# Kernel optimization log

Measured on AMD Instinct MI355X. Metric: run time of the kernel, lower is better.

## Reference

```python
import jax, jax.numpy as jnp
import numpy as np

B, L, C, H = 2, 4096, 512, 8
DH = C // H


def setup_inputs() -> dict:
    key = jax.random.key(0)
    ks = jax.random.split(key, 6)
    s = 1.0 / np.sqrt(C)
    return {
        "x": jax.random.normal(ks[0], (B, L, C), dtype=jnp.float32),
        "Wq": jax.random.normal(ks[1], (C, C), dtype=jnp.float32) * s,
        "Wk": jax.random.normal(ks[2], (C, C), dtype=jnp.float32) * s,
        "Wv": jax.random.normal(ks[3], (C, C), dtype=jnp.float32) * s,
        "Wo": jax.random.normal(ks[4], (C, C), dtype=jnp.float32) * s,
        "bo": jnp.zeros((C,), dtype=jnp.float32),
    }


def reference(x, Wq, Wk, Wv, Wo, bo):
    # x: [B, L, C]; split heads -> [B, H, L, Dh]
    def heads(t):
        return t.reshape(B, L, H, DH).transpose(0, 2, 1, 3)

    q = heads(x @ Wq)
    k = heads(x @ Wk)
    v = heads(x @ Wv)
    scale = 1.0 / np.sqrt(DH)
    scores = jnp.einsum("bhqd,bhkd->bhqk", q, k) * scale  # [B,H,L,L]
    w = jax.nn.softmax(scores, axis=-1)  # dropout_rate=0.0 -> identity
    att = jnp.einsum("bhqk,bhkd->bhqd", w, v)  # [B,H,L,Dh]
    att = att.transpose(0, 2, 1, 3).reshape(B, L, C)
    return att @ Wo + bo
```

## Files before the change

kernel.cpp:

```cpp
#include <hip/hip_runtime.h>
#include <hip/hip_bf16.h>

typedef __hip_bfloat16 bh;
typedef __attribute__((ext_vector_type(8))) __bf16 bf16x8;
typedef __attribute__((ext_vector_type(4))) float f32x4;
typedef __attribute__((ext_vector_type(4))) int i32x4;
typedef __attribute__((ext_vector_type(4))) short s16x4;

#define NB 2
#define NL 4096
#define NC 512
#define NH 8
#define NDH 64
#define NM (NB * NL)
#define LOG2E 1.4426950408889634f
#define KVBLK 8192

static __device__ __forceinline__ f32x4 mfma_bf16(bf16x8 a, bf16x8 b, f32x4 c) {
    return __builtin_amdgcn_mfma_f32_16x16x32_bf16(a, b, c, 0, 0, 0);
}
static __device__ __forceinline__ f32x4 mfma16(s16x4 a, s16x4 b, f32x4 c) {
    return __builtin_amdgcn_mfma_f32_16x16x16bf16_1k(a, b, c, 0, 0, 0);
}

static __device__ __forceinline__ void st_bf4(bh* dst, float a, float b, float c, float d) {
    bh tmp[4] = {__float2bfloat16(a), __float2bfloat16(b),
                 __float2bfloat16(c), __float2bfloat16(d)};
    *(s16x4*)dst = *(const s16x4*)tmp;
}
static __device__ __forceinline__ s16x4 pk_bf4(float a, float b, float c, float d) {
    bh tmp[4] = {__float2bfloat16(a), __float2bfloat16(b),
                 __float2bfloat16(c), __float2bfloat16(d)};
    return *(const s16x4*)tmp;
}

static __device__ __forceinline__ void gload16(const bh* g, bh* l) {
    __builtin_amdgcn_global_load_lds(
        (const __attribute__((address_space(1))) void*)g,
        (__attribute__((address_space(3))) void*)l,
        16, 0, 0);
}

__global__ __launch_bounds__(256, 2)
void prep(const float* __restrict__ x,
          const float* __restrict__ Wq, const float* __restrict__ Wk,
          const float* __restrict__ Wv, const float* __restrict__ Wo,
          bh* __restrict__ xf, bh* __restrict__ Wf)
{
    const int t = threadIdx.x;
    const int wave = t >> 6, lane = t & 63;
    const int quad = lane >> 4, c16 = lane & 15;

    if (blockIdx.z < 8) {
        __shared__ __align__(16) bh T[64][72];
        const int m64 = blockIdx.x, k64 = blockIdx.z;
        #pragma unroll
        for (int rep = 0; rep < 4; rep++) {
            int li = t + rep * 256;
            int r = li >> 4, c4 = (li & 15) * 4;
            float4 f = *(const float4*)&x[(size_t)(m64 * 64 + r) * 512 + k64 * 64 + c4];
            st_bf4(&T[r][c4], f.x, f.y, f.z, f.w);
        }
        __syncthreads();
        #pragma unroll
        for (int kcl = 0; kcl < 2; kcl++) {
            i32x4 v = *(const i32x4*)&T[wave * 16 + c16][kcl * 32 + quad * 8];
            size_t addr = ((size_t)(m64 * 4 + wave) * 16 + (k64 * 2 + kcl)) * 512 + lane * 8;
            *(i32x4*)&xf[addr] = v;
        }
    } else {
        if (blockIdx.x >= 64) return;
        int task = blockIdx.x * 4 + wave;
        int z = task >> 6, nt = (task >> 3) & 7, k0i = task & 7;
        const float* W = (z == 0) ? Wq : (z == 1) ? Wk : (z == 2) ? Wv : Wo;
        bh* dst = Wf + (((size_t)z * 8 + nt) * 8 + k0i) * 4096;
        #pragma unroll
        for (int kc = 0; kc < 2; kc++)
            #pragma unroll
            for (int fn = 0; fn < 4; fn++) {
                bh tmp[8];
                #pragma unroll
                for (int j = 0; j < 8; j++)
                    tmp[j] = __float2bfloat16(
                        W[(size_t)(k0i * 64 + kc * 32 + quad * 8 + j) * 512
                          + nt * 64 + fn * 16 + c16]);
                *(i32x4*)&dst[(kc * 4 + fn) * 512 + lane * 8] = *(const i32x4*)tmp;
            }
    }
}

__global__ __launch_bounds__(256, 2)
void qkv_gemm(const bh* __restrict__ xf, const bh* __restrict__ Wf,
              bh* __restrict__ Qb, bh* __restrict__ KVf)
{
    __shared__ __align__(16) bh smem[2][20480];

    const int t = threadIdx.x;
    const int wave = t >> 6, lane = t & 63;
    const int quad = lane >> 4, c16 = lane & 15;
    const int m0 = blockIdx.x * 128;
    const int nt = blockIdx.y;
    const int m16b = m0 >> 4;

    f32x4 acc[3][2][4];
    for (int z = 0; z < 3; z++)
        for (int a = 0; a < 2; a++)
            for (int b = 0; b < 4; b++)
                for (int u = 0; u < 4; u++) acc[z][a][b][u] = 0.0f;

    auto stage = [&](int k0i, int buf) {
        bh* Xl = &smem[buf][0];
        bh* Wl = &smem[buf][8192];
        #pragma unroll
        for (int r = 0; r < 4; r++) {
            int f = wave * 4 + r;
            const bh* src = xf + ((size_t)(m16b + (f >> 1)) * 16 + k0i * 2 + (f & 1)) * 512
                          + lane * 8;
            gload16(src, &Xl[f * 512 + lane * 8]);
        }
        #pragma unroll
        for (int z = 0; z < 3; z++) {
            const bh* wz = Wf + (((size_t)z * 8 + nt) * 8 + k0i) * 4096;
            #pragma unroll
            for (int r = 0; r < 2; r++) {
                int off = (wave * 2 + r) * 512 + lane * 8;
                gload16(wz + off, &Wl[z * 4096 + off]);
            }
        }
    };

    stage(0, 0);
    for (int k0i = 0; k0i < 8; k0i++) {
        const int buf = k0i & 1;
        __syncthreads();
        if (k0i < 7) stage(k0i + 1, buf ^ 1);
        const bh* Xl = &smem[buf][0];
        const bh* Wl = &smem[buf][8192];
        #pragma unroll
        for (int kc = 0; kc < 2; kc++) {
            bf16x8 af0 = *(const bf16x8*)&Xl[((wave * 2 + 0) * 2 + kc) * 512 + lane * 8];
            bf16x8 af1 = *(const bf16x8*)&Xl[((wave * 2 + 1) * 2 + kc) * 512 + lane * 8];
            #pragma unroll
            for (int z = 0; z < 3; z++)
                #pragma unroll
                for (int fn = 0; fn < 4; fn++) {
                    bf16x8 bf = *(const bf16x8*)&Wl[z * 4096 + (kc * 4 + fn) * 512 + lane * 8];
                    acc[z][0][fn] = mfma_bf16(af0, bf, acc[z][0][fn]);
                    acc[z][1][fn] = mfma_bf16(af1, bf, acc[z][1][fn]);
                }
        }
        __syncthreads();
    }

    const int h = nt;
    const int b = m0 >> 12;
    const int l0 = m0 & 4095;
    const int bh_i = b * NH + h;
    const int kt0 = l0 >> 6;

    {
        bh* Tq = &smem[0][0];
        #pragma unroll
        for (int fm = 0; fm < 2; fm++)
            #pragma unroll
            for (int i = 0; i < 4; i++) {
                int ll = wave * 32 + fm * 16 + quad * 4 + i;
                #pragma unroll
                for (int fn = 0; fn < 4; fn++)
                    Tq[ll * 68 + fn * 16 + c16] =
                        __float2bfloat16(acc[0][fm][fn][i] * 0.125f);
            }
        __syncthreads();
        int l = t >> 1, half = t & 1;
        bh* dst = Qb + ((size_t)bh_i * NL + l0 + l) * NDH + half * 32;
        const bh* src = &Tq[l * 68 + half * 32];
        #pragma unroll
        for (int r = 0; r < 4; r++)
            *(i32x4*)(dst + r * 8) = *(const i32x4*)(src + r * 8);
        __syncthreads();
    }

    {
        bh* Tk = &smem[0][0];
        #pragma unroll
        for (int fm = 0; fm < 2; fm++)
            #pragma unroll
            for (int i = 0; i < 4; i++) {
                int ll = wave * 32 + fm * 16 + quad * 4 + i;
                int ktl = ll >> 6, l64 = ll & 63;
                int fk = l64 >> 4, c16t = l64 & 15;
                #pragma unroll
                for (int fn = 0; fn < 4; fn++) {
                    int d = fn * 16 + c16;
                    int kc = d >> 5, qt = (d >> 3) & 3, j = d & 7;
                    Tk[ktl * 4096 + (fk * 2 + kc) * 512 + (qt * 16 + c16t) * 8 + j] =
                        __float2bfloat16(acc[1][fm][fn][i] * LOG2E);
                }
            }
        __syncthreads();
        int idx = t * 32;
        int ktl = idx >> 12, wi = idx & 4095;
        bh* dst = KVf + (size_t)(bh_i * 64 + kt0 + ktl) * KVBLK + wi;
        #pragma unroll
        for (int r = 0; r < 4; r++)
            *(i32x4*)(dst + r * 8) = *(const i32x4*)&Tk[idx + r * 8];
    }

    #pragma unroll
    for (int fm = 0; fm < 2; fm++) {
        int fkv = (wave * 2 + fm) & 3;
        int ktv = kt0 + (wave >> 1);
        #pragma unroll
        for (int fn = 0; fn < 4; fn++) {
            size_t addr = (size_t)(bh_i * 64 + ktv) * KVBLK + 4096
                        + (size_t)(fn * 4 + fkv) * 256 + (quad * 16 + c16) * 4;
            st_bf4(&KVf[addr], acc[2][fm][fn][0], acc[2][fm][fn][1],
                               acc[2][fm][fn][2], acc[2][fm][fn][3]);
        }
    }
}

__global__ __launch_bounds__(512, 4)
void flash_attn(const bh* __restrict__ Qb, const bh* __restrict__ KVf,
                bh* __restrict__ attb)
{
    __shared__ __align__(16) bh SF[2][2][KVBLK];

    const int t = threadIdx.x;
    const int wave = t >> 6, lane = t & 63;
    const int group = wave >> 2, w4 = wave & 3;
    const int quad = lane >> 4, c16 = lane & 15;
    const int bh_idx = blockIdx.y;
    const int q0 = blockIdx.x * 128;

    const bh* Qp  = Qb + (size_t)bh_idx * NL * NDH;
    const bh* KVp = KVf + (size_t)bh_idx * 64 * KVBLK;

    bf16x8 qf[2][2];
    #pragma unroll
    for (int fq = 0; fq < 2; fq++)
        #pragma unroll
        for (int kc = 0; kc < 2; kc++)
            qf[fq][kc] = *(const bf16x8*)
                &Qp[(size_t)(q0 + w4 * 32 + fq * 16 + c16) * NDH + kc * 32 + quad * 8];

    f32x4 ot[4][2];
    float lsum[2] = {0.0f, 0.0f};
    for (int a = 0; a < 4; a++)
        for (int fq = 0; fq < 2; fq++)
            for (int u = 0; u < 4; u++) ot[a][fq][u] = 0.0f;
    const f32x4 z4 = {0.0f, 0.0f, 0.0f, 0.0f};

    auto stage = [&](int i, int buf) {
        int kt = 2 * i + group;
        #pragma unroll
        for (int r = 0; r < 4; r++) {
            int off = (w4 * 4 + r) * 512 + lane * 8;
            gload16(KVp + (size_t)kt * KVBLK + off, &SF[group][buf][off]);
        }
    };

    stage(0, 0);
    for (int i = 0; i < 32; i++) {
        const int buf = i & 1;
        __syncthreads();
        if (i < 31) stage(i + 1, buf ^ 1);
        const bh* sf = &SF[group][buf][0];

        f32x4 s[4][2];
        #pragma unroll
        for (int fk = 0; fk < 4; fk++) {
            bf16x8 kf0 = *(const bf16x8*)&sf[(fk * 2 + 0) * 512 + lane * 8];
            s[fk][0] = mfma_bf16(kf0, qf[0][0], z4);
            s[fk][1] = mfma_bf16(kf0, qf[1][0], z4);
        }
        #pragma unroll
        for (int fk = 0; fk < 4; fk++) {
            bf16x8 kf1 = *(const bf16x8*)&sf[(fk * 2 + 1) * 512 + lane * 8];
            s[fk][0] = mfma_bf16(kf1, qf[0][1], s[fk][0]);
            s[fk][1] = mfma_bf16(kf1, qf[1][1], s[fk][1]);
        }

        s16x4 vt[4][4];
        #pragma unroll
        for (int fn = 0; fn < 4; fn++)
            #pragma unroll
            for (int fk = 0; fk < 4; fk++)
                vt[fn][fk] = *(const s16x4*)&sf[4096 + (fn * 4 + fk) * 256 + lane * 4];

        s16x4 pf[4][2];
        float rs0 = 0.0f, rs1 = 0.0f;
        #pragma unroll
        for (int fk = 0; fk < 4; fk++) {
            float a0 = __builtin_amdgcn_exp2f(s[fk][0][0]);
            float a1 = __builtin_amdgcn_exp2f(s[fk][0][1]);
            float a2 = __builtin_amdgcn_exp2f(s[fk][0][2]);
            float a3 = __builtin_amdgcn_exp2f(s[fk][0][3]);
            rs0 += (a0 + a1) + (a2 + a3);
            pf[fk][0] = pk_bf4(a0, a1, a2, a3);
            float b0 = __builtin_amdgcn_exp2f(s[fk][1][0]);
            float b1 = __builtin_amdgcn_exp2f(s[fk][1][1]);
            float b2 = __builtin_amdgcn_exp2f(s[fk][1][2]);
            float b3 = __builtin_amdgcn_exp2f(s[fk][1][3]);
            rs1 += (b0 + b1) + (b2 + b3);
            pf[fk][1] = pk_bf4(b0, b1, b2, b3);
        }
        lsum[0] += rs0;
        lsum[1] += rs1;

        #pragma unroll
        for (int fk = 0; fk < 4; fk++)
            #pragma unroll
            for (int fn = 0; fn < 4; fn++) {
                ot[fn][0] = mfma16(vt[fn][fk], pf[fk][0], ot[fn][0]);
                ot[fn][1] = mfma16(vt[fn][fk], pf[fk][1], ot[fn][1]);
            }
    }

    #pragma unroll
    for (int fq = 0; fq < 2; fq++) {
        lsum[fq] += __shfl_xor(lsum[fq], 16);
        lsum[fq] += __shfl_xor(lsum[fq], 32);
    }

    float* Ocmb = (float*)&SF[0][0][0];
    float* Lcmb = Ocmb + 128 * 64;
    __syncthreads();
    if (group == 1) {
        #pragma unroll
        for (int fq = 0; fq < 2; fq++) {
            int q = w4 * 32 + fq * 16 + c16;
            #pragma unroll
            for (int fn = 0; fn < 4; fn++)
                *(f32x4*)&Ocmb[q * 64 + fn * 16 + quad * 4] = ot[fn][fq];
            if (quad == 0) Lcmb[q] = lsum[fq];
        }
    }
    __syncthreads();
    if (group == 0) {
        const int b = bh_idx >> 3, h = bh_idx & 7;
        const int mbase16 = (b * NL + q0) >> 4;
        #pragma unroll
        for (int fq = 0; fq < 2; fq++) {
            int q = w4 * 32 + fq * 16 + c16;
            float inv = 1.0f / (lsum[fq] + Lcmb[q]);
            int m16 = mbase16 + w4 * 2 + fq;
            #pragma unroll
            for (int fn = 0; fn < 4; fn++) {
                f32x4 o2 = *(const f32x4*)&Ocmb[q * 64 + fn * 16 + quad * 4];
                size_t addr = ((size_t)m16 * 16 + h * 2 + (fn >> 1)) * 512
                            + (size_t)(((fn & 1) * 2 + (quad >> 1)) * 16 + c16) * 8
                            + (quad & 1) * 4;
                st_bf4(&attb[addr],
                       (ot[fn][fq][0] + o2[0]) * inv, (ot[fn][fq][1] + o2[1]) * inv,
                       (ot[fn][fq][2] + o2[2]) * inv, (ot[fn][fq][3] + o2[3]) * inv);
            }
        }
    }
}

__global__ __launch_bounds__(256, 2)
void out_gemm(const bh* __restrict__ Af, const bh* __restrict__ Wf,
              const float* __restrict__ bo, float* __restrict__ out)
{
    __shared__ __align__(16) bh smem[2][12288];

    const int t = threadIdx.x;
    const int wave = t >> 6, lane = t & 63;
    const int quad = lane >> 4, c16 = lane & 15;
    const int m0 = blockIdx.x * 128;
    const int nt = blockIdx.y;
    const int n0 = nt * 64;
    const int m16b = m0 >> 4;

    f32x4 acc[2][4];
    for (int a = 0; a < 2; a++)
        for (int b = 0; b < 4; b++)
            for (int u = 0; u < 4; u++) acc[a][b][u] = 0.0f;

    auto stage = [&](int k0i, int buf) {
        bh* Xl = &smem[buf][0];
        bh* Wl = &smem[buf][8192];
        #pragma unroll
        for (int r = 0; r < 4; r++) {
            int f = wave * 4 + r;
            const bh* src = Af + ((size_t)(m16b + (f >> 1)) * 16 + k0i * 2 + (f & 1)) * 512
                          + lane * 8;
            gload16(src, &Xl[f * 512 + lane * 8]);
        }
        const bh* wz = Wf + (((size_t)3 * 8 + nt) * 8 + k0i) * 4096;
        #pragma unroll
        for (int r = 0; r < 2; r++) {
            int off = (wave * 2 + r) * 512 + lane * 8;
            gload16(wz + off, &Wl[off]);
        }
    };

    stage(0, 0);
    for (int k0i = 0; k0i < 8; k0i++) {
        const int buf = k0i & 1;
        __syncthreads();
        if (k0i < 7) stage(k0i + 1, buf ^ 1);
        const bh* Xl = &smem[buf][0];
        const bh* Wl = &smem[buf][8192];
        #pragma unroll
        for (int kc = 0; kc < 2; kc++) {
            bf16x8 af0 = *(const bf16x8*)&Xl[((wave * 2 + 0) * 2 + kc) * 512 + lane * 8];
            bf16x8 af1 = *(const bf16x8*)&Xl[((wave * 2 + 1) * 2 + kc) * 512 + lane * 8];
            #pragma unroll
            for (int fn = 0; fn < 4; fn++) {
                bf16x8 bf = *(const bf16x8*)&Wl[(kc * 4 + fn) * 512 + lane * 8];
                acc[0][fn] = mfma_bf16(af0, bf, acc[0][fn]);
                acc[1][fn] = mfma_bf16(af1, bf, acc[1][fn]);
            }
        }
        __syncthreads();
    }

    #pragma unroll
    for (int fm = 0; fm < 2; fm++)
        #pragma unroll
        for (int i = 0; i < 4; i++) {
            int mr = m0 + wave * 32 + fm * 16 + quad * 4 + i;
            #pragma unroll
            for (int fn = 0; fn < 4; fn++) {
                int cn = n0 + fn * 16 + c16;
                out[(size_t)mr * 512 + cn] = acc[fm][fn][i] + bo[cn];
            }
        }
}

extern "C" void kernel_launch(void* const* d_in, const int* in_sizes, int n_in,
                              void* d_out, int out_size, void* d_ws, size_t ws_size,
                              hipStream_t stream)
{
    const float* x  = (const float*)d_in[0];
    const float* Wq = (const float*)d_in[1];
    const float* Wk = (const float*)d_in[2];
    const float* Wv = (const float*)d_in[3];
    const float* Wo = (const float*)d_in[4];
    const float* bo = (const float*)d_in[5];
    float* out = (float*)d_out;

    const size_t mat = (size_t)NM * NC;
    bh* Qb   = (bh*)d_ws;
    bh* KVf  = Qb + mat;
    bh* attb = KVf + 2 * mat;
    bh* Wf   = attb + mat;
    bh* xf   = Wf + 4 * 8 * 8 * 4096;

    prep      <<<dim3(128, 1, 9),         256, 0, stream>>>(x, Wq, Wk, Wv, Wo, xf, Wf);
    qkv_gemm  <<<dim3(NM / 128, NC / 64), 256, 0, stream>>>(xf, Wf, Qb, KVf);
    flash_attn<<<dim3(NL / 128, NB * NH), 512, 0, stream>>>(Qb, KVf, attb);
    out_gemm  <<<dim3(NM / 128, NC / 64), 256, 0, stream>>>(attb, Wf, bo, out);
}
```

Measured before the change: 186.5 us.

## Software-pipeline QK and PV across iterations with split K/V staging

Restructures the flash attention main loop so the PV MFMAs for tile i-1 interleave with the QK MFMAs and exp of tile i. K and V are now staged separately with their own double buffers, V loaded one iteration later than K, and P fragments ping-pong between two register sets. Wave priority is raised around the compute sections. This aims to hide exp/VALU latency behind MFMA work and shorten the serial dependency chain, at the cost of more live registers and a more complex prologue and epilogue.

```diff
diff --git a/kernel.cpp b/kernel.cpp
--- a/kernel.cpp
+++ b/kernel.cpp
@@ -224,7 +224,7 @@
 void flash_attn(const bh* __restrict__ Qb, const bh* __restrict__ KVf,
                 bh* __restrict__ attb)
 {
-    __shared__ __align__(16) bh SF[2][2][KVBLK];
+    __shared__ __align__(16) bh SMEM[32768];
 
     const int t = threadIdx.x;
     const int wave = t >> 6, lane = t & 63;
@@ -236,6 +236,9 @@
     const bh* Qp  = Qb + (size_t)bh_idx * NL * NDH;
     const bh* KVp = KVf + (size_t)bh_idx * 64 * KVBLK;
 
+    bh* Kb = &SMEM[group * 8192];
+    bh* Vb = &SMEM[16384 + group * 8192];
+
     bf16x8 qf[2][2];
     #pragma unroll
     for (int fq = 0; fq < 2; fq++)
@@ -251,70 +254,93 @@
             for (int u = 0; u < 4; u++) ot[a][fq][u] = 0.0f;
     const f32x4 z4 = {0.0f, 0.0f, 0.0f, 0.0f};
 
-    auto stage = [&](int i, int buf) {
+    s16x4 pfA[4][2], pfB[4][2];
+
+    auto stageK = [&](int i) {
         int kt = 2 * i + group;
-        #pragma unroll
-        for (int r = 0; r < 4; r++) {
-            int off = (w4 * 4 + r) * 512 + lane * 8;
-            gload16(KVp + (size_t)kt * KVBLK + off, &SF[group][buf][off]);
+        const bh* src = KVp + (size_t)kt * KVBLK;
+        bh* dst = Kb + (i & 1) * 4096;
+        #pragma unroll
+        for (int r = 0; r < 2; r++) {
+            int off = (w4 * 2 + r) * 512 + lane * 8;
+            gload16(src + off, dst + off);
         }
     };
-
-    stage(0, 0);
-    for (int i = 0; i < 32; i++) {
-        const int buf = i & 1;
-        __syncthreads();
-        if (i < 31) stage(i + 1, buf ^ 1);
-        const bh* sf = &SF[group][buf][0];
-
-        f32x4 s[4][2];
+    auto stageV = [&](int i) {
+        int kt = 2 * i + group;
+        const bh* src = KVp + (size_t)kt * KVBLK + 4096;
+        bh* dst = Vb + (i & 1) * 4096;
+        #pragma unroll
+        for (int r = 0; r < 2; r++) {
+            int off = (w4 * 2 + r) * 512 + lane * 8;
+            gload16(src + off, dst + off);
+        }
+    };
+
+    auto body = [&](int i, s16x4 (&pfC)[4][2], s16x4 (&pfP)[4][2],
+                    bool doPV, bool last) {
+        __syncthreads();
+        if (!last) stageK(i + 1);
+        stageV(i);
+        const bh* sfK = Kb + (i & 1) * 4096;
+        const bh* sfV = Vb + ((i + 1) & 1) * 4096;
+        __builtin_amdgcn_s_setprio(1);
+        float rs0 = 0.0f, rs1 = 0.0f;
         #pragma unroll
         for (int fk = 0; fk < 4; fk++) {
-            bf16x8 kf0 = *(const bf16x8*)&sf[(fk * 2 + 0) * 512 + lane * 8];
-            s[fk][0] = mfma_bf16(kf0, qf[0][0], z4);
-            s[fk][1] = mfma_bf16(kf0, qf[1][0], z4);
-        }
-        #pragma unroll
-        for (int fk = 0; fk < 4; fk++) {
-            bf16x8 kf1 = *(const bf16x8*)&sf[(fk * 2 + 1) * 512 + lane * 8];
-            s[fk][0] = mfma_bf16(kf1, qf[0][1], s[fk][0]);
-            s[fk][1] = mfma_bf16(kf1, qf[1][1], s[fk][1]);
-        }
-
-        s16x4 vt[4][4];
-        #pragma unroll
-        for (int fn = 0; fn < 4; fn++)
-            #pragma unroll
-            for (int fk = 0; fk < 4; fk++)
-                vt[fn][fk] = *(const s16x4*)&sf[4096 + (fn * 4 + fk) * 256 + lane * 4];
-
-        s16x4 pf[4][2];
-        float rs0 = 0.0f, rs1 = 0.0f;
-        #pragma unroll
-        for (int fk = 0; fk < 4; fk++) {
-            float a0 = __builtin_amdgcn_exp2f(s[fk][0][0]);
-            float a1 = __builtin_amdgcn_exp2f(s[fk][0][1]);
-            float a2 = __builtin_amdgcn_exp2f(s[fk][0][2]);
-            float a3 = __builtin_amdgcn_exp2f(s[fk][0][3]);
+            bf16x8 kf0 = *(const bf16x8*)&sfK[(fk * 2 + 0) * 512 + lane * 8];
+            bf16x8 kf1 = *(const bf16x8*)&sfK[(fk * 2 + 1) * 512 + lane * 8];
+            f32x4 s0 = mfma_bf16(kf0, qf[0][0], z4);
+            f32x4 s1 = mfma_bf16(kf0, qf[1][0], z4);
+            s0 = mfma_bf16(kf1, qf[0][1], s0);
+            s1 = mfma_bf16(kf1, qf[1][1], s1);
+            if (doPV) {
+                #pragma unroll
+                for (int fn = 0; fn < 4; fn++) {
+                    s16x4 vt = *(const s16x4*)&sfV[(fn * 4 + fk) * 256 + lane * 4];
+                    ot[fn][0] = mfma16(vt, pfP[fk][0], ot[fn][0]);
+                    ot[fn][1] = mfma16(vt, pfP[fk][1], ot[fn][1]);
+                }
+            }
+            float a0 = __builtin_amdgcn_exp2f(s0[0]);
+            float a1 = __builtin_amdgcn_exp2f(s0[1]);
+            float a2 = __builtin_amdgcn_exp2f(s0[2]);
+            float a3 = __builtin_amdgcn_exp2f(s0[3]);
             rs0 += (a0 + a1) + (a2 + a3);
-            pf[fk][0] = pk_bf4(a0, a1, a2, a3);
-            float b0 = __builtin_amdgcn_exp2f(s[fk][1][0]);
-            float b1 = __builtin_amdgcn_exp2f(s[fk][1][1]);
-            float b2 = __builtin_amdgcn_exp2f(s[fk][1][2]);
-            float b3 = __builtin_amdgcn_exp2f(s[fk][1][3]);
+            pfC[fk][0] = pk_bf4(a0, a1, a2, a3);
+            float b0 = __builtin_amdgcn_exp2f(s1[0]);
+            float b1 = __builtin_amdgcn_exp2f(s1[1]);
+            float b2 = __builtin_amdgcn_exp2f(s1[2]);
+            float b3 = __builtin_amdgcn_exp2f(s1[3]);
             rs1 += (b0 + b1) + (b2 + b3);
-            pf[fk][1] = pk_bf4(b0, b1, b2, b3);
+            pfC[fk][1] = pk_bf4(b0, b1, b2, b3);
         }
         lsum[0] += rs0;
         lsum[1] += rs1;
-
+        __builtin_amdgcn_s_setprio(0);
+    };
+
+    stageK(0);
+    body(0, pfA, pfB, false, false);
+    for (int i = 1; i < 31; i += 2) {
+        body(i,     pfB, pfA, true, false);
+        body(i + 1, pfA, pfB, true, false);
+    }
+    body(31, pfB, pfA, true, true);
+
+    __syncthreads();
+    {
+        const bh* sfV = Vb + 4096;
+        __builtin_amdgcn_s_setprio(1);
         #pragma unroll
         for (int fk = 0; fk < 4; fk++)
             #pragma unroll
             for (int fn = 0; fn < 4; fn++) {
-                ot[fn][0] = mfma16(vt[fn][fk], pf[fk][0], ot[fn][0]);
-                ot[fn][1] = mfma16(vt[fn][fk], pf[fk][1], ot[fn][1]);
-            }
+                s16x4 vt = *(const s16x4*)&sfV[(fn * 4 + fk) * 256 + lane * 4];
+                ot[fn][0] = mfma16(vt, pfB[fk][0], ot[fn][0]);
+                ot[fn][1] = mfma16(vt, pfB[fk][1], ot[fn][1]);
+            }
+        __builtin_amdgcn_s_setprio(0);
     }
 
     #pragma unroll
@@ -323,7 +349,7 @@
         lsum[fq] += __shfl_xor(lsum[fq], 32);
     }
 
-    float* Ocmb = (float*)&SF[0][0][0];
+    float* Ocmb = (float*)&SMEM[0];
     float* Lcmb = Ocmb + 128 * 64;
     __syncthreads();
     if (group == 1) {
```

After: 237.6 us. +27.4%, slower.
